# Kernel optimization log

Measured on AMD Instinct MI355X. Metric: run time of the kernel, lower is better.

## Reference

```python
import jax, jax.numpy as jnp
import numpy as np

N_NODES = 100000
N_RADIAL = 16  # columns 0..15
N_CONICAL = 16  # columns 16..31


def setup_inputs() -> dict:
    key = jax.random.key(0)
    k1, k2, k3, k4 = jax.random.split(key, 4)
    x = jax.random.normal(k1, (N_NODES, 32), dtype=jnp.float32)
    edge_index = jax.random.randint(k2, (2, 1600000), 0, N_NODES, dtype=jnp.int32)
    W1 = jax.random.normal(k3, (32, 128), dtype=jnp.float32) * 0.1
    b1 = jnp.zeros((128,), dtype=jnp.float32)
    W2 = jax.random.normal(k4, (128, 32), dtype=jnp.float32) * 0.1
    b2 = jnp.zeros((32,), dtype=jnp.float32)
    return {"x": x, "edge_index": edge_index, "W1": W1, "b1": b1, "W2": W2, "b2": b2}


def reference(x, edge_index, W1, b1, W2, b2):
    # slice radial / conical feature channels
    radial = x[:, :N_RADIAL]            # [N, 16]
    conical = x[:, N_RADIAL:N_RADIAL + N_CONICAL]  # [N, 16]

    i, j = edge_index[0], edge_index[1]
    rows = jnp.concatenate([i, j])      # symmetrized COO rows [2E]
    cols = jnp.concatenate([j, i])      # symmetrized COO cols [2E]

    # coalesce()+sparse.mm == segment-sum over all (duplicated) entries
    neighbor_sum = jax.ops.segment_sum(conical[cols], rows, num_segments=N_NODES)  # [N, 16]
    deg = jax.ops.segment_sum(jnp.ones_like(rows, dtype=x.dtype), rows, num_segments=N_NODES)
    deg = jnp.clip(deg, 1.0)[:, None]   # bincount(...).clamp(min=1)
    agg = neighbor_sum / deg            # mean aggregation

    combined = jnp.concatenate([radial, agg], axis=1)  # [N, 32]
    h = jax.nn.relu(combined @ W1 + b1)
    out = h @ W2 + b2                   # [N, 32]
    return out
```

## Files before the change

kernel.cpp:

```cpp
#include <hip/hip_runtime.h>
#include <hip/hip_fp16.h>

#define N_NODES  100000
#define N_RADIAL 16
#define N_CONICAL 16

#define NPB    256
#define NBKT   ((N_NODES + NPB - 1) / NPB)
#define NBLK_A 500
#define BTHR   512
#define CHUNK  6400
#define BINSTRIDE 6400
#define CAP    10240

typedef _Float16 h2vec __attribute__((ext_vector_type(2)));
static __device__ __forceinline__ float fdot2(__half2 a, __half2 b, float c) {
    h2vec av, bv;
    __builtin_memcpy(&av, &a, 4);
    __builtin_memcpy(&bv, &b, 4);
    return __builtin_amdgcn_fdot2(av, bv, c, false);
}

__global__ __launch_bounds__(BTHR) void binfuse_kernel(
    const int* __restrict__ idx, const float* __restrict__ x,
    __half2* __restrict__ xcon2,
    const float* __restrict__ W1, const float* __restrict__ W2,
    float* __restrict__ W1tr, __half* __restrict__ W1th, __half* __restrict__ W2th,
    unsigned int* __restrict__ binned, int* __restrict__ cnts,
    int* __restrict__ offs, int total, int E) {
    int b = blockIdx.x, tid = threadIdx.x;
    if (b >= NBLK_A) {
        int pb = b - NBLK_A;
        if (pb == 0) {
            for (int i = tid; i < 2048; i += BTHR) {
                int k = i >> 4, c = i & 15;
                W1tr[k * 16 + c] = W1[c * 128 + k];
                W1th[k * 16 + c] = __float2half(W1[(16 + c) * 128 + k]);
            }
            for (int i = tid; i < 4096; i += BTHR) {
                int kk = i >> 5, o = i & 31;
                W2th[o * 128 + kk] = __float2half(W2[i]);
            }
        } else {
            int t = (pb - 1) * BTHR + tid;
            if (t < N_NODES * 4) {
                int n = t >> 2, p = t & 3;
                float4 v = *((const float4*)(x + (size_t)n * 32 + 16) + p);
                __half2 h0 = __floats2half2_rn(v.x, v.y);
                __half2 h1 = __floats2half2_rn(v.z, v.w);
                uint2 st;
                st.x = *(unsigned int*)&h0; st.y = *(unsigned int*)&h1;
                *(uint2*)(xcon2 + 2 * t) = st;
            }
        }
        return;
    }

    __shared__ int cnt[NBKT];
    __shared__ int loff[NBKT];
    __shared__ unsigned int stage[CHUNK];
    for (int i = tid; i < NBKT; i += BTHR) cnt[i] = 0;
    __syncthreads();

    int lo = b * CHUNK;
    int cofs = (lo >= E) ? -E : E;
    const int4* rp = (const int4*)(idx + lo);
    const int4* cp = (const int4*)(idx + lo + cofs);
    int nq = CHUNK >> 2;

    #pragma unroll 1
    for (int q = tid; q < nq; q += BTHR) {
        int4 r = rp[q];
        atomicAdd(&cnt[r.x >> 8], 1);
        atomicAdd(&cnt[r.y >> 8], 1);
        atomicAdd(&cnt[r.z >> 8], 1);
        atomicAdd(&cnt[r.w >> 8], 1);
    }
    __syncthreads();

    if (tid < 64) {
        int c[7]; int s = 0;
        #pragma unroll
        for (int u = 0; u < 7; u++) {
            int i = tid * 7 + u;
            c[u] = (i < NBKT) ? cnt[i] : 0;
            s += c[u];
        }
        int t = s;
        #pragma unroll
        for (int off = 1; off < 64; off <<= 1) {
            int u = __shfl_up(t, off, 64);
            if (tid >= off) t += u;
        }
        int ex = t - s;
        #pragma unroll
        for (int u = 0; u < 7; u++) {
            int i = tid * 7 + u;
            if (i < NBKT) { loff[i] = ex; ex += c[u]; }
        }
    }
    __syncthreads();

    for (int i = tid; i < NBKT; i += BTHR) {
        cnts[i * NBLK_A + b] = cnt[i];
        offs[i * NBLK_A + b] = loff[i];
    }
    __syncthreads();

    #pragma unroll 1
    for (int q = tid; q < nq; q += BTHR) {
        int4 r = rp[q];
        int4 c = cp[q];
        int p0 = atomicAdd(&loff[r.x >> 8], 1);
        int p1 = atomicAdd(&loff[r.y >> 8], 1);
        int p2 = atomicAdd(&loff[r.z >> 8], 1);
        int p3 = atomicAdd(&loff[r.w >> 8], 1);
        stage[p0] = ((unsigned int)(r.x & 255) << 17) | (unsigned int)c.x;
        stage[p1] = ((unsigned int)(r.y & 255) << 17) | (unsigned int)c.y;
        stage[p2] = ((unsigned int)(r.z & 255) << 17) | (unsigned int)c.z;
        stage[p3] = ((unsigned int)(r.w & 255) << 17) | (unsigned int)c.w;
    }
    __syncthreads();

    unsigned int* dst = binned + (size_t)b * BINSTRIDE;
    for (int i = tid; i < CHUNK; i += BTHR) dst[i] = stage[i];
}

__global__ __launch_bounds__(1024, 2) void agg_kernel(
    const __half* __restrict__ xcon, const int* __restrict__ cnts,
    const int* __restrict__ offs,
    const unsigned int* __restrict__ binned, __half* __restrict__ agg) {
    __shared__ unsigned int sedge[CAP];
    __shared__ int scnt[NPB];
    __shared__ int soff[NPB];
    int orig = blockIdx.x;
    int xcd = orig & 7, i8 = orig >> 3;
    const int qq = NBKT >> 3, rr = NBKT & 7;
    int b = (xcd < rr) ? xcd * (qq + 1) + i8
                       : rr * (qq + 1) + (xcd - rr) * qq + i8;
    int tid = threadIdx.x;
    if (tid < NPB) scnt[tid] = 0;
    __syncthreads();

    int sub = tid >> 1, l = tid & 1;
    int sc = 0; unsigned int base = 0;
    if (sub < NBLK_A) {
        sc   = cnts[b * NBLK_A + sub];
        base = (unsigned int)sub * BINSTRIDE
             + (unsigned int)offs[b * NBLK_A + sub];
    }

    unsigned int ev[12];
    #pragma unroll
    for (int u = 0; u < 12; u++) {
        int j = l + 2 * u;
        ev[u] = 0u;
        if (j < sc) {
            ev[u] = binned[base + j];
            atomicAdd(&scnt[ev[u] >> 17], 1);
        }
    }
    for (int j = l + 24; j < sc; j += 2)
        atomicAdd(&scnt[binned[base + j] >> 17], 1);
    __syncthreads();

    if (tid < 64) {
        int i0 = tid * 4;
        int c0 = scnt[i0], c1 = scnt[i0 + 1], c2 = scnt[i0 + 2], c3 = scnt[i0 + 3];
        int s = c0 + c1 + c2 + c3;
        int t = s;
        #pragma unroll
        for (int off = 1; off < 64; off <<= 1) {
            int u = __shfl_up(t, off, 64);
            if (tid >= off) t += u;
        }
        int ex = t - s;
        soff[i0]     = ex;
        soff[i0 + 1] = ex + c0;
        soff[i0 + 2] = ex + c0 + c1;
        soff[i0 + 3] = ex + c0 + c1 + c2;
    }
    __syncthreads();

    #pragma unroll
    for (int u = 0; u < 12; u++) {
        int j = l + 2 * u;
        if (j < sc) {
            unsigned int p = ev[u];
            int pos = atomicAdd(&soff[p >> 17], 1);
            sedge[pos] = p & 0x1FFFFu;
        }
    }
    for (int j = l + 24; j < sc; j += 2) {
        unsigned int p = binned[base + j];
        int pos = atomicAdd(&soff[p >> 17], 1);
        sedge[pos] = p & 0x1FFFFu;
    }
    __syncthreads();

    if (tid < 2 * NPB) {
        int nl = tid >> 1, q = tid & 1;
        int c  = scnt[nl];
        int s0 = soff[nl] - c;
        float a0 = 0.f, a1 = 0.f, a2 = 0.f, a3 = 0.f;
        float a4 = 0.f, a5 = 0.f, a6 = 0.f, a7 = 0.f;
        #pragma unroll 2
        for (int k = 0; k < c; k++) {
            int col = (int)sedge[s0 + k];
            uint4 raw = ((const uint4*)(xcon + (size_t)col * 16))[q];
            float2 f0 = __half22float2(*(const __half2*)&raw.x);
            float2 f1 = __half22float2(*(const __half2*)&raw.y);
            float2 f2 = __half22float2(*(const __half2*)&raw.z);
            float2 f3 = __half22float2(*(const __half2*)&raw.w);
            a0 += f0.x; a1 += f0.y; a2 += f1.x; a3 += f1.y;
            a4 += f2.x; a5 += f2.y; a6 += f3.x; a7 += f3.y;
        }
        int n = b * NPB + nl;
        if (n < N_NODES) {
            float inv = 1.0f / (float)max(c, 1);
            __half2 h0 = __floats2half2_rn(a0 * inv, a1 * inv);
            __half2 h1 = __floats2half2_rn(a2 * inv, a3 * inv);
            __half2 h2 = __floats2half2_rn(a4 * inv, a5 * inv);
            __half2 h3 = __floats2half2_rn(a6 * inv, a7 * inv);
            uint4 st;
            st.x = *(unsigned int*)&h0; st.y = *(unsigned int*)&h1;
            st.z = *(unsigned int*)&h2; st.w = *(unsigned int*)&h3;
            *(uint4*)(agg + (size_t)n * 16 + q * 8) = st;
        }
    }
}

__global__ __launch_bounds__(512, 4) void mlp_kernel(
    const float* __restrict__ x, const __half* __restrict__ agg,
    const float* __restrict__ W1tr, const __half* __restrict__ W1th,
    const float* __restrict__ b1,
    const __half* __restrict__ W2th, const float* __restrict__ b2,
    float* __restrict__ out, int N) {
    __shared__ __half2 H2[64 * 64];
    int tid  = threadIdx.x;
    int lane = tid & 63;
    int ws   = __builtin_amdgcn_readfirstlane(tid >> 6);
    int n    = blockIdx.x * 64 + lane;
    int nc   = min(n, N - 1);

    float combr[16];
    const float4* xr = (const float4*)(x + (size_t)nc * 32);
    #pragma unroll
    for (int c = 0; c < 4; c++) {
        float4 v = xr[c];
        combr[c*4+0] = v.x; combr[c*4+1] = v.y;
        combr[c*4+2] = v.z; combr[c*4+3] = v.w;
    }
    __half2 aggh[8];
    const __half2* ar = (const __half2*)(agg + (size_t)nc * 16);
    #pragma unroll
    for (int c = 0; c < 8; c++) aggh[c] = ar[c];

    #pragma unroll
    for (int i = 0; i < 16; i += 2) {
        int k0 = ws * 16 + i;
        const float*   w1a  = W1tr + k0 * 16;
        const float*   w1b  = w1a + 16;
        const __half2* w1ha = (const __half2*)(W1th + k0 * 16);
        const __half2* w1hb = w1ha + 8;
        float ha = b1[k0], hb = b1[k0 + 1];
        #pragma unroll
        for (int c = 0; c < 16; c++) {
            ha = fmaf(combr[c], w1a[c], ha);
            hb = fmaf(combr[c], w1b[c], hb);
        }
        #pragma unroll
        for (int p = 0; p < 8; p++) {
            ha = fdot2(aggh[p], w1ha[p], ha);
            hb = fdot2(aggh[p], w1hb[p], hb);
        }
        ha = fmaxf(ha, 0.f); hb = fmaxf(hb, 0.f);
        H2[(k0 >> 1) * 64 + lane] = __floats2half2_rn(ha, hb);
    }
    __syncthreads();

    int o0 = ws * 4;
    const __half2* w20 = (const __half2*)(W2th + (o0 + 0) * 128);
    const __half2* w21 = (const __half2*)(W2th + (o0 + 1) * 128);
    const __half2* w22 = (const __half2*)(W2th + (o0 + 2) * 128);
    const __half2* w23 = (const __half2*)(W2th + (o0 + 3) * 128);
    float acc0 = b2[o0+0], acc1 = b2[o0+1], acc2 = b2[o0+2], acc3 = b2[o0+3];
    #pragma unroll 8
    for (int kp = 0; kp < 64; kp++) {
        __half2 hq = H2[kp * 64 + lane];
        acc0 = fdot2(hq, w20[kp], acc0);
        acc1 = fdot2(hq, w21[kp], acc1);
        acc2 = fdot2(hq, w22[kp], acc2);
        acc3 = fdot2(hq, w23[kp], acc3);
    }
    if (n < N) {
        float* op = out + (size_t)n * 32 + o0;
        op[0] = acc0; op[1] = acc1; op[2] = acc2; op[3] = acc3;
    }
}

extern "C" void kernel_launch(void* const* d_in, const int* in_sizes, int n_in,
                              void* d_out, int out_size, void* d_ws, size_t ws_size,
                              hipStream_t stream) {
    const float* x   = (const float*)d_in[0];
    const int*   idx = (const int*)d_in[1];
    const float* W1  = (const float*)d_in[2];
    const float* b1  = (const float*)d_in[3];
    const float* W2  = (const float*)d_in[4];
    const float* b2  = (const float*)d_in[5];
    float* out = (float*)d_out;

    const int E = in_sizes[1] / 2;
    const int total = 2 * E;

    char* base = (char*)d_ws;
    __half*       agg    = (__half*)base;
    __half*       xcon   = (__half*)(base + 3203072);
    float*        W1tr   = (float*)(base + 6406144);
    __half*       W1th   = (__half*)(base + 6414336);
    __half*       W2th   = (__half*)(base + 6418432);
    int*          cnts   = (int*)(base + 6426624);
    int*          offs   = (int*)(base + 7208960);
    unsigned int* binned = (unsigned int*)(base + 7991296);

    int pack_blocks = (N_NODES * 4 + BTHR - 1) / BTHR;
    binfuse_kernel<<<NBLK_A + 1 + pack_blocks, BTHR, 0, stream>>>(
        idx, x, (__half2*)xcon, W1, W2, W1tr, W1th, W2th,
        binned, cnts, offs, total, E);
    agg_kernel<<<NBKT, 1024, 0, stream>>>(xcon, cnts, offs, binned, agg);
    mlp_kernel<<<(N_NODES + 63) / 64, 512, 0, stream>>>(
        x, agg, W1tr, W1th, b1, W2th, b2, out, N_NODES);
}
```

Measured before the change: 139.9 us.

## Split aggregation buckets across two half-blocks and merge partials in MLP

```diff
diff --git a/kernel.cpp b/kernel.cpp
--- a/kernel.cpp
+++ b/kernel.cpp
@@ -11,7 +11,9 @@
 #define BTHR   512
 #define CHUNK  6400
 #define BINSTRIDE 6400
-#define CAP    10240
+#define HSUB   250
+#define CAP    5376
+#define ATHR   512
 
 typedef _Float16 h2vec __attribute__((ext_vector_type(2)));
 static __device__ __forceinline__ float fdot2(__half2 a, __half2 b, float c) {
@@ -126,15 +128,17 @@
     for (int i = tid; i < CHUNK; i += BTHR) dst[i] = stage[i];
 }
 
-__global__ __launch_bounds__(1024, 2) void agg_kernel(
+__global__ __launch_bounds__(ATHR, 8) void agg_kernel(
     const __half* __restrict__ xcon, const int* __restrict__ cnts,
     const int* __restrict__ offs,
-    const unsigned int* __restrict__ binned, __half* __restrict__ agg) {
+    const unsigned int* __restrict__ binned,
+    __half* __restrict__ aggp, unsigned short* __restrict__ degp) {
     __shared__ unsigned int sedge[CAP];
     __shared__ int scnt[NPB];
     __shared__ int soff[NPB];
     int orig = blockIdx.x;
-    int xcd = orig & 7, i8 = orig >> 3;
+    int bl   = orig >> 1, h = orig & 1;
+    int xcd = bl & 7, i8 = bl >> 3;
     const int qq = NBKT >> 3, rr = NBKT & 7;
     int b = (xcd < rr) ? xcd * (qq + 1) + i8
                        : rr * (qq + 1) + (xcd - rr) * qq + i8;
@@ -142,9 +146,9 @@
     if (tid < NPB) scnt[tid] = 0;
     __syncthreads();
 
-    int sub = tid >> 1, l = tid & 1;
+    int sub = h * HSUB + (tid >> 1), l = tid & 1;
     int sc = 0; unsigned int base = 0;
-    if (sub < NBLK_A) {
+    if ((tid >> 1) < HSUB) {
         sc   = cnts[b * NBLK_A + sub];
         base = (unsigned int)sub * BINSTRIDE
              + (unsigned int)offs[b * NBLK_A + sub];
@@ -198,7 +202,7 @@
     }
     __syncthreads();
 
-    if (tid < 2 * NPB) {
+    {
         int nl = tid >> 1, q = tid & 1;
         int c  = scnt[nl];
         int s0 = soff[nl] - c;
@@ -217,21 +221,22 @@
         }
         int n = b * NPB + nl;
         if (n < N_NODES) {
-            float inv = 1.0f / (float)max(c, 1);
-            __half2 h0 = __floats2half2_rn(a0 * inv, a1 * inv);
-            __half2 h1 = __floats2half2_rn(a2 * inv, a3 * inv);
-            __half2 h2 = __floats2half2_rn(a4 * inv, a5 * inv);
-            __half2 h3 = __floats2half2_rn(a6 * inv, a7 * inv);
+            __half2 h0 = __floats2half2_rn(a0, a1);
+            __half2 h1 = __floats2half2_rn(a2, a3);
+            __half2 h2 = __floats2half2_rn(a4, a5);
+            __half2 h3 = __floats2half2_rn(a6, a7);
             uint4 st;
             st.x = *(unsigned int*)&h0; st.y = *(unsigned int*)&h1;
             st.z = *(unsigned int*)&h2; st.w = *(unsigned int*)&h3;
-            *(uint4*)(agg + (size_t)n * 16 + q * 8) = st;
+            *(uint4*)(aggp + ((size_t)h * N_NODES + n) * 16 + q * 8) = st;
+            if (q == 0) degp[h * N_NODES + n] = (unsigned short)c;
         }
     }
 }
 
 __global__ __launch_bounds__(512, 4) void mlp_kernel(
-    const float* __restrict__ x, const __half* __restrict__ agg,
+    const float* __restrict__ x,
+    const __half* __restrict__ aggp, const unsigned short* __restrict__ degp,
     const float* __restrict__ W1tr, const __half* __restrict__ W1th,
     const float* __restrict__ b1,
     const __half* __restrict__ W2th, const float* __restrict__ b2,
@@ -252,9 +257,19 @@
         combr[c*4+2] = v.z; combr[c*4+3] = v.w;
     }
     __half2 aggh[8];
-    const __half2* ar = (const __half2*)(agg + (size_t)nc * 16);
-    #pragma unroll
-    for (int c = 0; c < 8; c++) aggh[c] = ar[c];
+    {
+        const __half2* A0 = (const __half2*)(aggp + (size_t)nc * 16);
+        const __half2* A1 = (const __half2*)(aggp + ((size_t)N_NODES + nc) * 16);
+        int d = (int)degp[nc] + (int)degp[N_NODES + nc];
+        float inv = 1.0f / (float)max(d, 1);
+        #pragma unroll
+        for (int p = 0; p < 8; p++) {
+            float2 f0 = __half22float2(A0[p]);
+            float2 f1 = __half22float2(A1[p]);
+            aggh[p] = __floats2half2_rn((f0.x + f1.x) * inv,
+                                        (f0.y + f1.y) * inv);
+        }
+    }
 
     #pragma unroll
     for (int i = 0; i < 16; i += 2) {
@@ -314,20 +329,22 @@
     const int total = 2 * E;
 
     char* base = (char*)d_ws;
-    __half*       agg    = (__half*)base;
-    __half*       xcon   = (__half*)(base + 3203072);
-    float*        W1tr   = (float*)(base + 6406144);
-    __half*       W1th   = (__half*)(base + 6414336);
-    __half*       W2th   = (__half*)(base + 6418432);
-    int*          cnts   = (int*)(base + 6426624);
-    int*          offs   = (int*)(base + 7208960);
-    unsigned int* binned = (unsigned int*)(base + 7991296);
+    __half*         aggp   = (__half*)base;
+    __half*         xcon   = (__half*)(base + 6406144);
+    float*          W1tr   = (float*)(base + 9609216);
+    __half*         W1th   = (__half*)(base + 9617408);
+    __half*         W2th   = (__half*)(base + 9621504);
+    unsigned short* degp   = (unsigned short*)(base + 9629696);
+    int*            cnts   = (int*)(base + 10030080);
+    int*            offs   = (int*)(base + 10812416);
+    unsigned int*   binned = (unsigned int*)(base + 11594752);
 
     int pack_blocks = (N_NODES * 4 + BTHR - 1) / BTHR;
     binfuse_kernel<<<NBLK_A + 1 + pack_blocks, BTHR, 0, stream>>>(
         idx, x, (__half2*)xcon, W1, W2, W1tr, W1th, W2th,
         binned, cnts, offs, total, E);
-    agg_kernel<<<NBKT, 1024, 0, stream>>>(xcon, cnts, offs, binned, agg);
+    agg_kernel<<<NBKT * 2, ATHR, 0, stream>>>(
+        xcon, cnts, offs, binned, aggp, degp);
     mlp_kernel<<<(N_NODES + 63) / 64, 512, 0, stream>>>(
-        x, agg, W1tr, W1th, b1, W2th, b2, out, N_NODES);
-}
+        x, aggp, degp, W1tr, W1th, b1, W2th, b2, out, N_NODES);
+}
```

Measured after the change: 144.8 us. 3.5% more time.
